# Kernel tuning notes

Hardware: AMD Instinct MI355X
Metric: run time of the kernel (lower is better)

Reference implementation:

```python
import jax, jax.numpy as jnp
import numpy as np
from jax import lax

MU = 255
H = 64            # block_hidden_size
SKIP = 256        # skip_size
NUM_LAYERS = 24
CYCLE = 6
UP_CONV = 4       # upsample_convs=[4]
UP_REPEAT = 75
LF = 80           # local_features_size
B = 2
L = 64            # local feature frames
T = L * UP_CONV * UP_REPEAT  # 19200 signal samples


def setup_inputs() -> dict:
    key = jax.random.key(0)
    ks = jax.random.split(key, 16)
    r = lambda k, shape, sc=0.05: jax.random.normal(k, shape, jnp.float32) * sc
    return {
        "local_features": jax.random.normal(ks[0], (B, L, LF), jnp.float32),
        "gold_signal": jax.random.uniform(ks[1], (B, T), jnp.float32, minval=-1.0, maxval=1.0),
        "embed_w": r(ks[2], (H, 1)),
        "embed_b": r(ks[3], (H,)),
        "up_w": r(ks[4], (LF, LF, UP_CONV)),
        "up_b": r(ks[5], (LF,)),
        "proj_w": r(ks[6], (NUM_LAYERS * 2 * H, LF)),
        "proj_b": r(ks[7], (NUM_LAYERS * 2 * H,)),
        "dil_w": r(ks[8], (NUM_LAYERS, 2 * H, H, 2)),
        "dil_b": r(ks[9], (NUM_LAYERS, 2 * H)),
        "skip_w": r(ks[10], (NUM_LAYERS, SKIP, H)),
        "skip_b": r(ks[11], (NUM_LAYERS, SKIP)),
        "res_w": r(ks[12], (NUM_LAYERS - 1, H, H)),
        "res_b": r(ks[13], (NUM_LAYERS - 1, H)),
        "out1_w": r(ks[14], (MU + 1, SKIP)),
        "out2_w": r(ks[15], (MU + 1, MU + 1)),
    }


def _causal_dilated_conv(x, w, b, dilation):
    # x: [B, C, T]; w: [O, C, 2]; left-pad so output[t] depends on inputs <= t
    xp = jnp.pad(x, ((0, 0), (0, 0), (dilation, 0)))
    y = lax.conv_general_dilated(xp, w, window_strides=(1,), padding="VALID",
                                 rhs_dilation=(dilation,),
                                 dimension_numbers=("NCH", "OIH", "NCH"))
    return y + b[None, :, None]


def _upsample(local_features, up_w, up_b, proj_w, proj_b):
    # local_features: [B, L, LF] -> cond [B, NUM_LAYERS, 2H, T]
    x = jnp.transpose(local_features, (0, 2, 1))  # [B, LF, L]
    # ConvTranspose1d with kernel_size == stride == UP_CONV (no overlap)
    y = jnp.einsum("bfl,fgk->bglk", x, up_w).reshape(x.shape[0], LF, -1)
    y = y + up_b[None, :, None]                                  # [B, LF, L*4]
    # 1x1 projection to per-layer gate conditioning (chunking in the original
    # is a memory trick, math-identical to a single conv)
    z = jnp.einsum("bft,of->bot", y, proj_w) + proj_b[None, :, None]
    z = jnp.repeat(z, UP_REPEAT, axis=-1)                        # [B, NL*2H, T]
    return z.reshape(z.shape[0], NUM_LAYERS, 2 * H, -1)


def reference(local_features, gold_signal, embed_w, embed_b, up_w, up_b,
              proj_w, proj_b, dil_w, dil_b, skip_w, skip_b, res_w, res_b,
              out1_w, out2_w):
    cond = _upsample(local_features, up_w, up_b, proj_w, proj_b)
    # embed: Conv1d(1 -> H, kernel 1)
    x = gold_signal[:, None, :] * embed_w[None, :, :] + embed_b[None, :, None]
    skip_sum = None
    for i in range(NUM_LAYERS):
        dilation = 2 ** (i % CYCLE)
        y = _causal_dilated_conv(x, dil_w[i], dil_b[i], dilation) + cond[:, i]
        gated = jnp.tanh(y[:, :H]) * jax.nn.sigmoid(y[:, H:])
        skip = jnp.einsum("bht,sh->bst", gated, skip_w[i]) + skip_b[i][None, :, None]
        skip_sum = skip if skip_sum is None else skip_sum + skip
        if i < NUM_LAYERS - 1:  # last layer has no residual out_conv
            x = x + jnp.einsum("bht,oh->bot", gated, res_w[i]) + res_b[i][None, :, None]
    h = jnp.einsum("bst,os->bot", jax.nn.relu(skip_sum), out1_w)
    h = jnp.einsum("bst,os->bot", jax.nn.relu(h), out2_w)
    return jax.nn.log_softmax(h, axis=1)  # [B, MU+1, T]
```

## Files before the change

kernel.cpp:

```cpp
#include <hip/hip_runtime.h>
#include <math.h>

#define T_TOT 19200
#define HD    64
#define SKIPN 256
#define NLAYER 24
#define LFN   80
#define NB    2
#define NTL   128
#define HALO  64
#define XR    (NTL + HALO)
#define NGT   (T_TOT / NTL)
#define NOH   32
#define NTH   (T_TOT / NOH)
#define NCH   (T_TOT / 32)

typedef float  f32x4  __attribute__((ext_vector_type(4)));
typedef __bf16 bf16x8 __attribute__((ext_vector_type(8)));
typedef __bf16 bf16x4 __attribute__((ext_vector_type(4)));

__device__ __forceinline__ f32x4 mfma16(bf16x8 a, bf16x8 b, f32x4 c) {
    return __builtin_amdgcn_mfma_f32_16x16x32_bf16(a, b, c, 0, 0, 0);
}

__global__ __launch_bounds__(256) void prep_kernel(
    const float* __restrict__ dil_w, const float* __restrict__ skip_w,
    const float* __restrict__ skip_b, const float* __restrict__ res_w,
    const float* __restrict__ out1_w, const float* __restrict__ out2_w,
    __bf16* __restrict__ A1f, __bf16* __restrict__ Asf, __bf16* __restrict__ A3f,
    __bf16* __restrict__ Ao1f, __bf16* __restrict__ Ao2f, float* __restrict__ sbsum)
{
    int idx = blockIdx.x * 256 + threadIdx.x;
    if (idx < 24 * 128 * 128) {
        {
            int j = idx & 7, lane = (idx >> 3) & 63, ks = (idx >> 9) & 3;
            int mt = (idx >> 11) & 7, l = idx >> 14;
            int row = mt * 16 + (lane & 15);
            int k   = ks * 32 + (lane >> 4) * 8 + j;
            A1f[idx] = (__bf16)dil_w[((l * 128 + row) * 64 + (k & 63)) * 2 + (k >> 6)];
        }
        {
            int j = idx & 7, lane = (idx >> 3) & 63, ks = (idx >> 9) & 1;
            int mt = (idx >> 10) & 15, l = idx >> 14;
            int row = mt * 16 + (lane & 15);
            int k   = ks * 32 + (lane >> 4) * 8 + j;
            Asf[idx] = (__bf16)skip_w[(l * 256 + row) * 64 + k];
        }
    }
    if (idx < 23 * 64 * 64) {
        int j = idx & 7, lane = (idx >> 3) & 63, ks = (idx >> 9) & 1;
        int mt = (idx >> 10) & 3, l = idx >> 12;
        int row = mt * 16 + (lane & 15);
        int k   = ks * 32 + (lane >> 4) * 8 + j;
        A3f[idx] = (__bf16)res_w[(l * 64 + row) * 64 + k];
    }
    if (idx < 256 * 256) {
        int j = idx & 7, lane = (idx >> 3) & 63, ks = (idx >> 9) & 7;
        int mt = idx >> 12;
        int row = mt * 16 + (lane & 15);
        int k   = ks * 32 + (lane >> 4) * 8 + j;
        Ao1f[idx] = (__bf16)out1_w[row * 256 + k];
        Ao2f[idx] = (__bf16)out2_w[row * 256 + k];
    }
    if (idx < 256) {
        float s = 0.0f;
        #pragma unroll
        for (int l = 0; l < NLAYER; ++l) s += skip_b[l * 256 + idx];
        sbsum[idx] = s;
    }
}

__global__ __launch_bounds__(256) void up_kernel(
    const float* __restrict__ lf, const float* __restrict__ up_w,
    const float* __restrict__ up_b, float* __restrict__ y_up)
{
    int idx = blockIdx.x * 256 + threadIdx.x;
    if (idx >= NB * LFN * 256) return;
    int t4 = idx & 255;
    int g  = (idx >> 8) % LFN;
    int b  = idx / (LFN * 256);
    int l = t4 >> 2, k = t4 & 3;
    float acc = up_b[g];
    const float* lfp = lf + (b * 64 + l) * LFN;
    #pragma unroll 8
    for (int f = 0; f < LFN; ++f)
        acc += lfp[f] * up_w[(f * LFN + g) * 4 + k];
    y_up[idx] = acc;
}

__global__ __launch_bounds__(256) void proj_kernel(
    const float* __restrict__ y_up, const float* __restrict__ proj_w,
    const float* __restrict__ proj_b, float* __restrict__ z)
{
    int idx = blockIdx.x * 256 + threadIdx.x;
    if (idx >= NB * 3072 * 256) return;
    int t4 = idx & 255;
    int o  = (idx >> 8) % 3072;
    int b  = idx / (3072 * 256);
    float acc = proj_b[o];
    const float* yp = y_up + b * LFN * 256 + t4;
    const float* wp = proj_w + o * LFN;
    #pragma unroll 8
    for (int g = 0; g < LFN; ++g)
        acc += wp[g] * yp[g * 256];
    z[idx] = acc;
}

__global__ __launch_bounds__(512, 4) void layer_group(
    const float* __restrict__ gold, const float* __restrict__ ew,
    const float* __restrict__ eb,
    const __bf16* __restrict__ xg_in, __bf16* __restrict__ xg_out,
    const float* __restrict__ zbuf, const float* __restrict__ dil_b,
    const float* __restrict__ res_b,
    const __bf16* __restrict__ A1f, const __bf16* __restrict__ A3f,
    __bf16* __restrict__ G, int L0, int first, int last)
{
    __shared__ __bf16 xh[XR][72];
    __shared__ __bf16 Gs[XR][72];
    __shared__ float  zs[4][128];

    const int b    = blockIdx.y;
    const int tb   = blockIdx.x;
    const int t0   = tb * NTL;
    const int tid  = threadIdx.x;
    const int lane = tid & 63;
    const int w    = tid >> 6;
    const int wm   = w & 3;
    const int wg   = w >> 2;
    const int n16  = lane & 15;
    const int quad = lane >> 4;
    const int q0   = ((t0 - HALO > 0) ? t0 - HALO : 0) / 75;

    bf16x8 z8;
    #pragma unroll
    for (int u = 0; u < 8; ++u) z8[u] = (__bf16)0.0f;

    if (first) {
        for (int idx = tid; idx < XR * 8; idx += 512) {
            int r = idx >> 3, hc = (idx & 7) * 8;
            int t = t0 - HALO + r;
            bf16x8 v = z8;
            if (t >= 0) {
                float gv = gold[b * T_TOT + t];
                #pragma unroll
                for (int u = 0; u < 8; ++u)
                    v[u] = (__bf16)(gv * ew[hc + u] + eb[hc + u]);
            }
            *(bf16x8*)&xh[r][hc] = v;
        }
    } else {
        for (int idx = tid; idx < XR * 8; idx += 512) {
            int r = idx >> 3, hc = (idx & 7) * 8;
            int t = t0 - HALO + r;
            bf16x8 v = (t >= 0)
                ? *(const bf16x8*)&xg_in[((size_t)b * T_TOT + t) * 64 + hc] : z8;
            *(bf16x8*)&xh[r][hc] = v;
        }
    }

    const bf16x8* A1v = (const bf16x8*)A1f;
    const bf16x8* A3v = (const bf16x8*)A3f;
    f32x4 zero4 = {0.0f, 0.0f, 0.0f, 0.0f};

    for (int j = 0; j < 6; ++j) {
        const int l = L0 + j;
        const int d = 1 << j;

        if (tid < 512) {
            int qq = tid >> 7, o = tid & 127;
            int q = q0 + qq; if (q > 255) q = 255;
            zs[qq][o] = dil_b[l * 128 + o] +
                        zbuf[((size_t)(b * 3072 + l * 128 + o)) * 256 + q];
        }
        bf16x8 a1a[4], a1b[4];
        #pragma unroll
        for (int ks = 0; ks < 4; ++ks) {
            a1a[ks] = A1v[((l * 8 + wm) * 4 + ks) * 64 + lane];
            a1b[ks] = A1v[((l * 8 + 4 + wm) * 4 + ks) * 64 + lane];
        }
        __syncthreads();

        #pragma unroll
        for (int nt0 = 0; nt0 < 6; ++nt0) {
            int nt = wg * 6 + nt0;
            int nn = nt * 16 + n16;
            int rm = (nn >= d) ? nn - d : 0;
            bf16x8 b0 = *(const bf16x8*)&xh[rm][quad * 8];
            bf16x8 b1 = *(const bf16x8*)&xh[rm][32 + quad * 8];
            bf16x8 b2 = *(const bf16x8*)&xh[nn][quad * 8];
            bf16x8 b3 = *(const bf16x8*)&xh[nn][32 + quad * 8];
            f32x4 aa = zero4, ab = zero4;
            aa = mfma16(a1a[0], b0, aa); ab = mfma16(a1b[0], b0, ab);
            aa = mfma16(a1a[1], b1, aa); ab = mfma16(a1b[1], b1, ab);
            aa = mfma16(a1a[2], b2, aa); ab = mfma16(a1b[2], b2, ab);
            aa = mfma16(a1a[3], b3, aa); ab = mfma16(a1b[3], b3, ab);

            int tt = t0 - HALO + nn;
            int qq = ((tt > 0) ? tt : 0) / 75 - q0;
            bf16x4 g4;
            #pragma unroll
            for (int r = 0; r < 4; ++r) {
                int o = wm * 16 + quad * 4 + r;
                float ya = aa[r] + zs[qq][o];
                float yb = ab[r] + zs[qq][o + 64];
                float th = 1.0f - 2.0f * __builtin_amdgcn_rcpf(__expf(2.0f * ya) + 1.0f);
                float sg = __builtin_amdgcn_rcpf(1.0f + __expf(-yb));
                g4[r] = (__bf16)(th * sg);
            }
            *(bf16x4*)&Gs[nn][wm * 16 + quad * 4] = g4;
        }
        __syncthreads();

        {
            __bf16* Gl = G + (((size_t)(b * NCH + tb * 4)) * NLAYER + l) * 2048;
            for (int idx = tid; idx < 128 * 8; idx += 512) {
                int rr = idx >> 3, hc = (idx & 7) * 8;
                size_t off = (size_t)(rr >> 5) * (NLAYER * 2048) + (rr & 31) * 64 + hc;
                *(bf16x8*)&Gl[off] = *(const bf16x8*)&Gs[HALO + rr][hc];
            }
        }

        if (l < NLAYER - 1) {
            bf16x8 a3[2];
            #pragma unroll
            for (int ks = 0; ks < 2; ++ks)
                a3[ks] = A3v[((l * 4 + wm) * 2 + ks) * 64 + lane];
            int o0 = wm * 16 + quad * 4;
            f32x4 rb = *(const f32x4*)&res_b[l * 64 + o0];
            #pragma unroll
            for (int nt0 = 0; nt0 < 6; ++nt0) {
                int nn = (wg * 6 + nt0) * 16 + n16;
                bf16x8 g0 = *(const bf16x8*)&Gs[nn][quad * 8];
                bf16x8 g1 = *(const bf16x8*)&Gs[nn][32 + quad * 8];
                f32x4 ar = zero4;
                ar = mfma16(a3[0], g0, ar);
                ar = mfma16(a3[1], g1, ar);
                bf16x4 xo = *(const bf16x4*)&xh[nn][o0];
                bf16x4 xn;
                #pragma unroll
                for (int r = 0; r < 4; ++r)
                    xn[r] = (__bf16)((float)xo[r] + ar[r] + rb[r]);
                *(bf16x4*)&xh[nn][o0] = xn;
            }
        }
    }

    if (!last) {
        __syncthreads();
        for (int idx = tid; idx < 128 * 8; idx += 512) {
            int rr = idx >> 3, hc = (idx & 7) * 8;
            *(bf16x8*)&xg_out[((size_t)b * T_TOT + t0 + rr) * 64 + hc] =
                *(const bf16x8*)&xh[HALO + rr][hc];
        }
    }
}

__global__ __launch_bounds__(256, 4) void head_mfma(
    const __bf16* __restrict__ G, const __bf16* __restrict__ Asf,
    const float* __restrict__ sbsum, const __bf16* __restrict__ Ao1f,
    const __bf16* __restrict__ Ao2f, float* __restrict__ out)
{
    __shared__ __bf16 Vs[NOH][264];
    __shared__ float redm[4][2][16];
    __shared__ float reds[4][2][16];

    const int b    = blockIdx.y;
    const int tcb  = blockIdx.x;
    const int t0   = tcb * NOH;
    const int tid  = threadIdx.x;
    const int lane = tid & 63;
    const int w    = tid >> 6;
    const int n16  = lane & 15;
    const int quad = lane >> 4;

    f32x4 zero4 = {0.0f, 0.0f, 0.0f, 0.0f};
    f32x4 acc[4][2];
    #pragma unroll
    for (int mt = 0; mt < 4; ++mt)
        #pragma unroll
        for (int nt = 0; nt < 2; ++nt) acc[mt][nt] = zero4;

    const bf16x8* Asv = (const bf16x8*)Asf;
    const __bf16* Gc  = G + ((size_t)(b * NCH + tcb)) * (NLAYER * 2048);

    for (int l = 0; l < NLAYER; ++l) {
        const __bf16* Gl = Gc + l * 2048;
        #pragma unroll
        for (int ks = 0; ks < 2; ++ks) {
            bf16x8 bfr[2];
            #pragma unroll
            for (int nt = 0; nt < 2; ++nt)
                bfr[nt] = *(const bf16x8*)&Gl[(nt * 16 + n16) * 64 + ks * 32 + quad * 8];
            #pragma unroll
            for (int mt = 0; mt < 4; ++mt) {
                bf16x8 af = Asv[((l * 16 + w * 4 + mt) * 2 + ks) * 64 + lane];
                #pragma unroll
                for (int nt = 0; nt < 2; ++nt)
                    acc[mt][nt] = mfma16(af, bfr[nt], acc[mt][nt]);
            }
        }
    }
    {
        int s0 = w * 64 + quad * 4;
        #pragma unroll
        for (int mt = 0; mt < 4; ++mt)
            #pragma unroll
            for (int nt = 0; nt < 2; ++nt) {
                bf16x4 v4;
                #pragma unroll
                for (int r = 0; r < 4; ++r)
                    v4[r] = (__bf16)fmaxf(acc[mt][nt][r] + sbsum[s0 + mt * 16 + r], 0.0f);
                *(bf16x4*)&Vs[nt * 16 + n16][s0 + mt * 16] = v4;
            }
    }
    __syncthreads();

    const bf16x8* W1v = (const bf16x8*)Ao1f;
    const bf16x8* W2v = (const bf16x8*)Ao2f;

    #pragma unroll
    for (int mt = 0; mt < 4; ++mt)
        #pragma unroll
        for (int nt = 0; nt < 2; ++nt) acc[mt][nt] = zero4;
    #pragma unroll
    for (int ks = 0; ks < 8; ++ks) {
        bf16x8 bfr[2];
        #pragma unroll
        for (int nt = 0; nt < 2; ++nt)
            bfr[nt] = *(const bf16x8*)&Vs[nt * 16 + n16][ks * 32 + quad * 8];
        #pragma unroll
        for (int mt = 0; mt < 4; ++mt) {
            bf16x8 af = W1v[((w * 4 + mt) * 8 + ks) * 64 + lane];
            #pragma unroll
            for (int nt = 0; nt < 2; ++nt)
                acc[mt][nt] = mfma16(af, bfr[nt], acc[mt][nt]);
        }
    }
    __syncthreads();
    #pragma unroll
    for (int mt = 0; mt < 4; ++mt)
        #pragma unroll
        for (int nt = 0; nt < 2; ++nt) {
            int o0 = w * 64 + mt * 16 + quad * 4;
            bf16x4 v4;
            #pragma unroll
            for (int r = 0; r < 4; ++r)
                v4[r] = (__bf16)fmaxf(acc[mt][nt][r], 0.0f);
            *(bf16x4*)&Vs[nt * 16 + n16][o0] = v4;
        }
    __syncthreads();

    #pragma unroll
    for (int mt = 0; mt < 4; ++mt)
        #pragma unroll
        for (int nt = 0; nt < 2; ++nt) acc[mt][nt] = zero4;
    #pragma unroll
    for (int ks = 0; ks < 8; ++ks) {
        bf16x8 bfr[2];
        #pragma unroll
        for (int nt = 0; nt < 2; ++nt)
            bfr[nt] = *(const bf16x8*)&Vs[nt * 16 + n16][ks * 32 + quad * 8];
        #pragma unroll
        for (int mt = 0; mt < 4; ++mt) {
            bf16x8 af = W2v[((w * 4 + mt) * 8 + ks) * 64 + lane];
            #pragma unroll
            for (int nt = 0; nt < 2; ++nt)
                acc[mt][nt] = mfma16(af, bfr[nt], acc[mt][nt]);
        }
    }

    float lmax[2], lsum[2];
    #pragma unroll
    for (int nt = 0; nt < 2; ++nt) {
        float m = -1e30f;
        #pragma unroll
        for (int mt = 0; mt < 4; ++mt)
            #pragma unroll
            for (int r = 0; r < 4; ++r) m = fmaxf(m, acc[mt][nt][r]);
        m = fmaxf(m, __shfl_xor(m, 16, 64));
        m = fmaxf(m, __shfl_xor(m, 32, 64));
        lmax[nt] = m;
    }
    if (quad == 0) {
        #pragma unroll
        for (int nt = 0; nt < 2; ++nt) redm[w][nt][n16] = lmax[nt];
    }
    __syncthreads();
    #pragma unroll
    for (int nt = 0; nt < 2; ++nt) {
        float m = redm[0][nt][n16];
        m = fmaxf(m, redm[1][nt][n16]);
        m = fmaxf(m, redm[2][nt][n16]);
        m = fmaxf(m, redm[3][nt][n16]);
        lmax[nt] = m;
        float s = 0.0f;
        #pragma unroll
        for (int mt = 0; mt < 4; ++mt)
            #pragma unroll
            for (int r = 0; r < 4; ++r) s += __expf(acc[mt][nt][r] - m);
        s += __shfl_xor(s, 16, 64);
        s += __shfl_xor(s, 32, 64);
        lsum[nt] = s;
    }
    if (quad == 0) {
        #pragma unroll
        for (int nt = 0; nt < 2; ++nt) reds[w][nt][n16] = lsum[nt];
    }
    __syncthreads();
    #pragma unroll
    for (int nt = 0; nt < 2; ++nt) {
        float s = reds[0][nt][n16] + reds[1][nt][n16] +
                  reds[2][nt][n16] + reds[3][nt][n16];
        float lse = lmax[nt] + logf(s);
        int t = t0 + nt * 16 + n16;
        #pragma unroll
        for (int mt = 0; mt < 4; ++mt)
            #pragma unroll
            for (int r = 0; r < 4; ++r) {
                int o = w * 64 + mt * 16 + quad * 4 + r;
                out[((size_t)(b * SKIPN + o)) * T_TOT + t] = acc[mt][nt][r] - lse;
            }
    }
}

extern "C" void kernel_launch(void* const* d_in, const int* in_sizes, int n_in,
                              void* d_out, int out_size, void* d_ws, size_t ws_size,
                              hipStream_t stream) {
    const float* lf       = (const float*)d_in[0];
    const float* gold     = (const float*)d_in[1];
    const float* embed_w  = (const float*)d_in[2];
    const float* embed_b  = (const float*)d_in[3];
    const float* up_w     = (const float*)d_in[4];
    const float* up_b     = (const float*)d_in[5];
    const float* proj_w   = (const float*)d_in[6];
    const float* proj_b   = (const float*)d_in[7];
    const float* dil_w    = (const float*)d_in[8];
    const float* dil_b    = (const float*)d_in[9];
    const float* skip_w   = (const float*)d_in[10];
    const float* skip_b   = (const float*)d_in[11];
    const float* res_w    = (const float*)d_in[12];
    const float* res_b    = (const float*)d_in[13];
    const float* out1_w   = (const float*)d_in[14];
    const float* out2_w   = (const float*)d_in[15];

    __bf16* A1f  = (__bf16*)d_ws;
    __bf16* Asf  = A1f + 393216;
    __bf16* A3f  = Asf + 393216;
    __bf16* Ao1f = A3f + 94208;
    __bf16* Ao2f = Ao1f + 65536;
    __bf16* G    = Ao2f + 65536;
    __bf16* xga  = G + (size_t)NB * NCH * NLAYER * 2048;
    __bf16* xgb  = xga + (size_t)NB * T_TOT * HD;
    float*  sbsum = (float*)(xgb + (size_t)NB * T_TOT * HD);
    float*  y_up  = sbsum + 256;
    float*  zbuf  = y_up + NB * LFN * 256;

    prep_kernel<<<(24 * 128 * 128 + 255) / 256, 256, 0, stream>>>(
        dil_w, skip_w, skip_b, res_w, out1_w, out2_w,
        A1f, Asf, A3f, Ao1f, Ao2f, sbsum);
    up_kernel  <<<(NB * LFN * 256 + 255) / 256, 256, 0, stream>>>(lf, up_w, up_b, y_up);
    proj_kernel<<<(NB * 3072 * 256) / 256,      256, 0, stream>>>(y_up, proj_w, proj_b, zbuf);

    const __bf16* xin[4] = { xga, xga, xgb, xga };
    __bf16*       xout[4] = { xga, xgb, xga, xgb };
    for (int g = 0; g < 4; ++g) {
        layer_group<<<dim3(NGT, NB), 512, 0, stream>>>(
            gold, embed_w, embed_b, xin[g], xout[g],
            zbuf, dil_b, res_b, A1f, A3f, G,
            6 * g, (g == 0) ? 1 : 0, (g == 3) ? 1 : 0);
    }

    head_mfma<<<dim3(NTH, NB), 256, 0, stream>>>(G, Asf, sbsum, Ao1f, Ao2f, (float*)d_out);
}
```

Baseline: 382.5 us.

## Shrink layer tiles, skip unneeded halo rows, transpose conditioning, prefetch head G

Halves the time tile per layer block to 64 outputs with 256 threads, so there are more blocks. Each layer skips the halo row tiles that can no longer influence valid outputs, based on the cumulative dilation. A new transpose kernel pre-adds the dilation bias and stores conditioning as time-major, so the per-layer z loads are contiguous. The head kernel double-buffers G fragments across layers. The cost is a larger halo-to-output ratio, meaning more redundant halo compute per output row, plus one extra launch and buffer.

New measurement: 391.2 us. 2.3% more time.

```diff
diff --git a/kernel.cpp b/kernel.cpp
--- a/kernel.cpp
+++ b/kernel.cpp
@@ -7,7 +7,7 @@
 #define NLAYER 24
 #define LFN   80
 #define NB    2
-#define NTL   128
+#define NTL   64
 #define HALO  64
 #define XR    (NTL + HALO)
 #define NGT   (T_TOT / NTL)
@@ -106,18 +106,41 @@
     z[idx] = acc;
 }
 
-__global__ __launch_bounds__(512, 4) void layer_group(
+__global__ __launch_bounds__(256) void ztrans_kernel(
+    const float* __restrict__ z, const float* __restrict__ dil_b,
+    float* __restrict__ zt)
+{
+    __shared__ float tile[32][33];
+    const int b  = blockIdx.z;
+    const int o0 = blockIdx.x * 32;
+    const int q0 = blockIdx.y * 32;
+    const int tx = threadIdx.x & 31;
+    const int ty = threadIdx.x >> 5;
+    #pragma unroll
+    for (int k = 0; k < 4; ++k) {
+        int o = o0 + ty + k * 8;
+        tile[ty + k * 8][tx] = z[((size_t)(b * 3072 + o)) * 256 + q0 + tx];
+    }
+    __syncthreads();
+    #pragma unroll
+    for (int k = 0; k < 4; ++k) {
+        int q = q0 + ty + k * 8;
+        int o = o0 + tx;
+        zt[((size_t)(b * 256 + q)) * 3072 + o] = tile[tx][ty + k * 8] + dil_b[o];
+    }
+}
+
+__global__ __launch_bounds__(256, 3) void layer_group(
     const float* __restrict__ gold, const float* __restrict__ ew,
     const float* __restrict__ eb,
     const __bf16* __restrict__ xg_in, __bf16* __restrict__ xg_out,
-    const float* __restrict__ zbuf, const float* __restrict__ dil_b,
-    const float* __restrict__ res_b,
+    const float* __restrict__ zt, const float* __restrict__ res_b,
     const __bf16* __restrict__ A1f, const __bf16* __restrict__ A3f,
     __bf16* __restrict__ G, int L0, int first, int last)
 {
     __shared__ __bf16 xh[XR][72];
     __shared__ __bf16 Gs[XR][72];
-    __shared__ float  zs[4][128];
+    __shared__ float  zs[3][128];
 
     const int b    = blockIdx.y;
     const int tb   = blockIdx.x;
@@ -125,8 +148,6 @@
     const int tid  = threadIdx.x;
     const int lane = tid & 63;
     const int w    = tid >> 6;
-    const int wm   = w & 3;
-    const int wg   = w >> 2;
     const int n16  = lane & 15;
     const int quad = lane >> 4;
     const int q0   = ((t0 - HALO > 0) ? t0 - HALO : 0) / 75;
@@ -136,7 +157,7 @@
     for (int u = 0; u < 8; ++u) z8[u] = (__bf16)0.0f;
 
     if (first) {
-        for (int idx = tid; idx < XR * 8; idx += 512) {
+        for (int idx = tid; idx < XR * 8; idx += 256) {
             int r = idx >> 3, hc = (idx & 7) * 8;
             int t = t0 - HALO + r;
             bf16x8 v = z8;
@@ -149,7 +170,7 @@
             *(bf16x8*)&xh[r][hc] = v;
         }
     } else {
-        for (int idx = tid; idx < XR * 8; idx += 512) {
+        for (int idx = tid; idx < XR * 8; idx += 256) {
             int r = idx >> 3, hc = (idx & 7) * 8;
             int t = t0 - HALO + r;
             bf16x8 v = (t >= 0)
@@ -161,28 +182,26 @@
     const bf16x8* A1v = (const bf16x8*)A1f;
     const bf16x8* A3v = (const bf16x8*)A3f;
     f32x4 zero4 = {0.0f, 0.0f, 0.0f, 0.0f};
+    const int stj[6] = {0, 0, 0, 1, 2, 4};
 
     for (int j = 0; j < 6; ++j) {
         const int l = L0 + j;
         const int d = 1 << j;
 
-        if (tid < 512) {
-            int qq = tid >> 7, o = tid & 127;
+        for (int idx = tid; idx < 384; idx += 256) {
+            int qq = idx >> 7, oo = idx & 127;
             int q = q0 + qq; if (q > 255) q = 255;
-            zs[qq][o] = dil_b[l * 128 + o] +
-                        zbuf[((size_t)(b * 3072 + l * 128 + o)) * 256 + q];
+            zs[qq][oo] = zt[((size_t)(b * 256 + q)) * 3072 + l * 128 + oo];
         }
         bf16x8 a1a[4], a1b[4];
         #pragma unroll
         for (int ks = 0; ks < 4; ++ks) {
-            a1a[ks] = A1v[((l * 8 + wm) * 4 + ks) * 64 + lane];
-            a1b[ks] = A1v[((l * 8 + 4 + wm) * 4 + ks) * 64 + lane];
+            a1a[ks] = A1v[((l * 8 + w) * 4 + ks) * 64 + lane];
+            a1b[ks] = A1v[((l * 8 + 4 + w) * 4 + ks) * 64 + lane];
         }
         __syncthreads();
 
-        #pragma unroll
-        for (int nt0 = 0; nt0 < 6; ++nt0) {
-            int nt = wg * 6 + nt0;
+        for (int nt = stj[j]; nt < 8; ++nt) {
             int nn = nt * 16 + n16;
             int rm = (nn >= d) ? nn - d : 0;
             bf16x8 b0 = *(const bf16x8*)&xh[rm][quad * 8];
@@ -197,39 +216,38 @@
 
             int tt = t0 - HALO + nn;
             int qq = ((tt > 0) ? tt : 0) / 75 - q0;
+            int o0 = w * 16 + quad * 4;
+            f32x4 za = *(const f32x4*)&zs[qq][o0];
+            f32x4 zb = *(const f32x4*)&zs[qq][o0 + 64];
             bf16x4 g4;
             #pragma unroll
             for (int r = 0; r < 4; ++r) {
-                int o = wm * 16 + quad * 4 + r;
-                float ya = aa[r] + zs[qq][o];
-                float yb = ab[r] + zs[qq][o + 64];
+                float ya = aa[r] + za[r];
+                float yb = ab[r] + zb[r];
                 float th = 1.0f - 2.0f * __builtin_amdgcn_rcpf(__expf(2.0f * ya) + 1.0f);
                 float sg = __builtin_amdgcn_rcpf(1.0f + __expf(-yb));
                 g4[r] = (__bf16)(th * sg);
             }
-            *(bf16x4*)&Gs[nn][wm * 16 + quad * 4] = g4;
+            *(bf16x4*)&Gs[nn][o0] = g4;
         }
         __syncthreads();
 
-        {
-            __bf16* Gl = G + (((size_t)(b * NCH + tb * 4)) * NLAYER + l) * 2048;
-            for (int idx = tid; idx < 128 * 8; idx += 512) {
-                int rr = idx >> 3, hc = (idx & 7) * 8;
-                size_t off = (size_t)(rr >> 5) * (NLAYER * 2048) + (rr & 31) * 64 + hc;
-                *(bf16x8*)&Gl[off] = *(const bf16x8*)&Gs[HALO + rr][hc];
-            }
+        for (int idx = tid; idx < 512; idx += 256) {
+            int rr = idx >> 3, hc = (idx & 7) * 8;
+            int cb = tb * 2 + (rr >> 5);
+            size_t off = ((size_t)(b * NCH + cb) * NLAYER + l) * 2048 + (rr & 31) * 64 + hc;
+            *(bf16x8*)&G[off] = *(const bf16x8*)&Gs[HALO + rr][hc];
         }
 
         if (l < NLAYER - 1) {
             bf16x8 a3[2];
             #pragma unroll
             for (int ks = 0; ks < 2; ++ks)
-                a3[ks] = A3v[((l * 4 + wm) * 2 + ks) * 64 + lane];
-            int o0 = wm * 16 + quad * 4;
+                a3[ks] = A3v[((l * 4 + w) * 2 + ks) * 64 + lane];
+            int o0 = w * 16 + quad * 4;
             f32x4 rb = *(const f32x4*)&res_b[l * 64 + o0];
-            #pragma unroll
-            for (int nt0 = 0; nt0 < 6; ++nt0) {
-                int nn = (wg * 6 + nt0) * 16 + n16;
+            for (int nt = stj[j]; nt < 8; ++nt) {
+                int nn = nt * 16 + n16;
                 bf16x8 g0 = *(const bf16x8*)&Gs[nn][quad * 8];
                 bf16x8 g1 = *(const bf16x8*)&Gs[nn][32 + quad * 8];
                 f32x4 ar = zero4;
@@ -247,7 +265,7 @@
 
     if (!last) {
         __syncthreads();
-        for (int idx = tid; idx < 128 * 8; idx += 512) {
+        for (int idx = tid; idx < 512; idx += 256) {
             int rr = idx >> 3, hc = (idx & 7) * 8;
             *(bf16x8*)&xg_out[((size_t)b * T_TOT + t0 + rr) * 64 + hc] =
                 *(const bf16x8*)&xh[HALO + rr][hc];
@@ -281,24 +299,34 @@
         for (int nt = 0; nt < 2; ++nt) acc[mt][nt] = zero4;
 
     const bf16x8* Asv = (const bf16x8*)Asf;
-    const __bf16* Gc  = G + ((size_t)(b * NCH + tcb)) * (NLAYER * 2048);
-
+    const __bf16* Gl  = G + ((size_t)(b * NCH + tcb)) * (NLAYER * 2048);
+
+    bf16x8 gb[4], gn[4];
+    #pragma unroll
+    for (int p = 0; p < 4; ++p) {
+        int ks = p >> 1, nt = p & 1;
+        gb[p] = *(const bf16x8*)&Gl[(nt * 16 + n16) * 64 + ks * 32 + quad * 8];
+    }
     for (int l = 0; l < NLAYER; ++l) {
-        const __bf16* Gl = Gc + l * 2048;
-        #pragma unroll
-        for (int ks = 0; ks < 2; ++ks) {
-            bf16x8 bfr[2];
-            #pragma unroll
-            for (int nt = 0; nt < 2; ++nt)
-                bfr[nt] = *(const bf16x8*)&Gl[(nt * 16 + n16) * 64 + ks * 32 + quad * 8];
+        if (l < NLAYER - 1) {
+            const __bf16* Gn = Gl + 2048;
+            #pragma unroll
+            for (int p = 0; p < 4; ++p) {
+                int ks = p >> 1, nt = p & 1;
+                gn[p] = *(const bf16x8*)&Gn[(nt * 16 + n16) * 64 + ks * 32 + quad * 8];
+            }
+        }
+        #pragma unroll
+        for (int ks = 0; ks < 2; ++ks)
             #pragma unroll
             for (int mt = 0; mt < 4; ++mt) {
                 bf16x8 af = Asv[((l * 16 + w * 4 + mt) * 2 + ks) * 64 + lane];
-                #pragma unroll
-                for (int nt = 0; nt < 2; ++nt)
-                    acc[mt][nt] = mfma16(af, bfr[nt], acc[mt][nt]);
-            }
-        }
+                acc[mt][0] = mfma16(af, gb[ks * 2 + 0], acc[mt][0]);
+                acc[mt][1] = mfma16(af, gb[ks * 2 + 1], acc[mt][1]);
+            }
+        #pragma unroll
+        for (int p = 0; p < 4; ++p) gb[p] = gn[p];
+        Gl += 2048;
     }
     {
         int s0 = w * 64 + quad * 4;
@@ -453,20 +481,22 @@
     __bf16* xgb  = xga + (size_t)NB * T_TOT * HD;
     float*  sbsum = (float*)(xgb + (size_t)NB * T_TOT * HD);
     float*  y_up  = sbsum + 256;
-    float*  zbuf  = y_up + NB * LFN * 256;
+    float*  z     = y_up + NB * LFN * 256;
+    float*  zt    = z + NB * 3072 * 256;
 
     prep_kernel<<<(24 * 128 * 128 + 255) / 256, 256, 0, stream>>>(
         dil_w, skip_w, skip_b, res_w, out1_w, out2_w,
         A1f, Asf, A3f, Ao1f, Ao2f, sbsum);
     up_kernel  <<<(NB * LFN * 256 + 255) / 256, 256, 0, stream>>>(lf, up_w, up_b, y_up);
-    proj_kernel<<<(NB * 3072 * 256) / 256,      256, 0, stream>>>(y_up, proj_w, proj_b, zbuf);
+    proj_kernel<<<(NB * 3072 * 256) / 256,      256, 0, stream>>>(y_up, proj_w, proj_b, z);
+    ztrans_kernel<<<dim3(96, 8, NB), 256, 0, stream>>>(z, dil_b, zt);
 
     const __bf16* xin[4] = { xga, xga, xgb, xga };
     __bf16*       xout[4] = { xga, xgb, xga, xgb };
     for (int g = 0; g < 4; ++g) {
-        layer_group<<<dim3(NGT, NB), 512, 0, stream>>>(
+        layer_group<<<dim3(NGT, NB), 256, 0, stream>>>(
             gold, embed_w, embed_b, xin[g], xout[g],
-            zbuf, dil_b, res_b, A1f, A3f, G,
+            zt, res_b, A1f, A3f, G,
             6 * g, (g == 0) ? 1 : 0, (g == 3) ? 1 : 0);
     }
 
```

## Transpose conditioning buffer and widen head tile to 64 timesteps with 8 waves

Applied to the files above, without the earlier changes.

Adds a transpose kernel that folds dil_b into the projected conditioning and stores it time-major, so layer_group's per-layer zs load becomes coalesced and the gate step reads it as vector loads. The head kernel now processes 64 timesteps per block with 512 threads, with each wave covering 2 M-tiles by 4 N-tiles. This halves the number of head blocks and reuses each weight fragment across more columns. The cost is an extra kernel launch, an extra transposed buffer, and fewer, larger head blocks with an 8-way reduction.

Result: slower. 443.2 us (+15.9%).

```diff
diff --git a/kernel.cpp b/kernel.cpp
--- a/kernel.cpp
+++ b/kernel.cpp
@@ -11,7 +11,7 @@
 #define HALO  64
 #define XR    (NTL + HALO)
 #define NGT   (T_TOT / NTL)
-#define NOH   32
+#define NOH   64
 #define NTH   (T_TOT / NOH)
 #define NCH   (T_TOT / 32)
 
@@ -106,12 +106,35 @@
     z[idx] = acc;
 }
 
+__global__ __launch_bounds__(256) void ztrans_kernel(
+    const float* __restrict__ z, const float* __restrict__ dil_b,
+    float* __restrict__ zt)
+{
+    __shared__ float tile[32][33];
+    const int b  = blockIdx.z;
+    const int o0 = blockIdx.x * 32;
+    const int q0 = blockIdx.y * 32;
+    const int tx = threadIdx.x & 31;
+    const int ty = threadIdx.x >> 5;
+    #pragma unroll
+    for (int k = 0; k < 4; ++k) {
+        int o = o0 + ty + k * 8;
+        tile[ty + k * 8][tx] = z[((size_t)(b * 3072 + o)) * 256 + q0 + tx];
+    }
+    __syncthreads();
+    #pragma unroll
+    for (int k = 0; k < 4; ++k) {
+        int q = q0 + ty + k * 8;
+        int o = o0 + tx;
+        zt[((size_t)(b * 256 + q)) * 3072 + o] = tile[tx][ty + k * 8] + dil_b[o];
+    }
+}
+
 __global__ __launch_bounds__(512, 4) void layer_group(
     const float* __restrict__ gold, const float* __restrict__ ew,
     const float* __restrict__ eb,
     const __bf16* __restrict__ xg_in, __bf16* __restrict__ xg_out,
-    const float* __restrict__ zbuf, const float* __restrict__ dil_b,
-    const float* __restrict__ res_b,
+    const float* __restrict__ zt, const float* __restrict__ res_b,
     const __bf16* __restrict__ A1f, const __bf16* __restrict__ A3f,
     __bf16* __restrict__ G, int L0, int first, int last)
 {
@@ -166,11 +189,10 @@
         const int l = L0 + j;
         const int d = 1 << j;
 
-        if (tid < 512) {
-            int qq = tid >> 7, o = tid & 127;
+        {
+            int qq = tid >> 7, oo = tid & 127;
             int q = q0 + qq; if (q > 255) q = 255;
-            zs[qq][o] = dil_b[l * 128 + o] +
-                        zbuf[((size_t)(b * 3072 + l * 128 + o)) * 256 + q];
+            zs[qq][oo] = zt[((size_t)(b * 256 + q)) * 3072 + l * 128 + oo];
         }
         bf16x8 a1a[4], a1b[4];
         #pragma unroll
@@ -197,17 +219,19 @@
 
             int tt = t0 - HALO + nn;
             int qq = ((tt > 0) ? tt : 0) / 75 - q0;
+            int o0 = wm * 16 + quad * 4;
+            f32x4 za = *(const f32x4*)&zs[qq][o0];
+            f32x4 zb = *(const f32x4*)&zs[qq][o0 + 64];
             bf16x4 g4;
             #pragma unroll
             for (int r = 0; r < 4; ++r) {
-                int o = wm * 16 + quad * 4 + r;
-                float ya = aa[r] + zs[qq][o];
-                float yb = ab[r] + zs[qq][o + 64];
+                float ya = aa[r] + za[r];
+                float yb = ab[r] + zb[r];
                 float th = 1.0f - 2.0f * __builtin_amdgcn_rcpf(__expf(2.0f * ya) + 1.0f);
                 float sg = __builtin_amdgcn_rcpf(1.0f + __expf(-yb));
                 g4[r] = (__bf16)(th * sg);
             }
-            *(bf16x4*)&Gs[nn][wm * 16 + quad * 4] = g4;
+            *(bf16x4*)&Gs[nn][o0] = g4;
         }
         __syncthreads();
 
@@ -255,18 +279,18 @@
     }
 }
 
-__global__ __launch_bounds__(256, 4) void head_mfma(
+__global__ __launch_bounds__(512, 2) void head_mfma(
     const __bf16* __restrict__ G, const __bf16* __restrict__ Asf,
     const float* __restrict__ sbsum, const __bf16* __restrict__ Ao1f,
     const __bf16* __restrict__ Ao2f, float* __restrict__ out)
 {
     __shared__ __bf16 Vs[NOH][264];
-    __shared__ float redm[4][2][16];
-    __shared__ float reds[4][2][16];
+    __shared__ float redm[8][4][16];
+    __shared__ float reds[8][4][16];
 
     const int b    = blockIdx.y;
-    const int tcb  = blockIdx.x;
-    const int t0   = tcb * NOH;
+    const int xb   = blockIdx.x;
+    const int t0   = xb * NOH;
     const int tid  = threadIdx.x;
     const int lane = tid & 63;
     const int w    = tid >> 6;
@@ -274,44 +298,49 @@
     const int quad = lane >> 4;
 
     f32x4 zero4 = {0.0f, 0.0f, 0.0f, 0.0f};
-    f32x4 acc[4][2];
-    #pragma unroll
-    for (int mt = 0; mt < 4; ++mt)
-        #pragma unroll
-        for (int nt = 0; nt < 2; ++nt) acc[mt][nt] = zero4;
+    f32x4 acc[2][4];
+    #pragma unroll
+    for (int mt = 0; mt < 2; ++mt)
+        #pragma unroll
+        for (int nt = 0; nt < 4; ++nt) acc[mt][nt] = zero4;
 
     const bf16x8* Asv = (const bf16x8*)Asf;
-    const __bf16* Gc  = G + ((size_t)(b * NCH + tcb)) * (NLAYER * 2048);
+    const __bf16* Gc0 = G + ((size_t)(b * NCH + xb * 2) * NLAYER) * 2048;
+    const __bf16* Gc1 = Gc0 + (size_t)NLAYER * 2048;
 
     for (int l = 0; l < NLAYER; ++l) {
-        const __bf16* Gl = Gc + l * 2048;
+        bf16x8 bfr[2][4];
         #pragma unroll
         for (int ks = 0; ks < 2; ++ks) {
-            bf16x8 bfr[2];
-            #pragma unroll
-            for (int nt = 0; nt < 2; ++nt)
-                bfr[nt] = *(const bf16x8*)&Gl[(nt * 16 + n16) * 64 + ks * 32 + quad * 8];
-            #pragma unroll
-            for (int mt = 0; mt < 4; ++mt) {
-                bf16x8 af = Asv[((l * 16 + w * 4 + mt) * 2 + ks) * 64 + lane];
+            #pragma unroll
+            for (int nt = 0; nt < 4; ++nt) {
+                const __bf16* base = ((nt < 2) ? Gc0 : Gc1) + l * 2048;
+                bfr[ks][nt] = *(const bf16x8*)
+                    &base[((nt & 1) * 16 + n16) * 64 + ks * 32 + quad * 8];
+            }
+        }
+        #pragma unroll
+        for (int ks = 0; ks < 2; ++ks)
+            #pragma unroll
+            for (int mt = 0; mt < 2; ++mt) {
+                bf16x8 af = Asv[((l * 16 + w * 2 + mt) * 2 + ks) * 64 + lane];
                 #pragma unroll
-                for (int nt = 0; nt < 2; ++nt)
-                    acc[mt][nt] = mfma16(af, bfr[nt], acc[mt][nt]);
-            }
-        }
-    }
-    {
-        int s0 = w * 64 + quad * 4;
-        #pragma unroll
-        for (int mt = 0; mt < 4; ++mt)
-            #pragma unroll
-            for (int nt = 0; nt < 2; ++nt) {
-                bf16x4 v4;
-                #pragma unroll
-                for (int r = 0; r < 4; ++r)
-                    v4[r] = (__bf16)fmaxf(acc[mt][nt][r] + sbsum[s0 + mt * 16 + r], 0.0f);
-                *(bf16x4*)&Vs[nt * 16 + n16][s0 + mt * 16] = v4;
-            }
+                for (int nt = 0; nt < 4; ++nt)
+                    acc[mt][nt] = mfma16(af, bfr[ks][nt], acc[mt][nt]);
+            }
+    }
+    #pragma unroll
+    for (int mt = 0; mt < 2; ++mt) {
+        int s0 = (w * 2 + mt) * 16 + quad * 4;
+        f32x4 sb = *(const f32x4*)&sbsum[s0];
+        #pragma unroll
+        for (int nt = 0; nt < 4; ++nt) {
+            bf16x4 v4;
+            #pragma unroll
+            for (int r = 0; r < 4; ++r)
+                v4[r] = (__bf16)fmaxf(acc[mt][nt][r] + sb[r], 0.0f);
+            *(bf16x4*)&Vs[nt * 16 + n16][s0] = v4;
+        }
     }
     __syncthreads();
 
@@ -319,62 +348,63 @@
     const bf16x8* W2v = (const bf16x8*)Ao2f;
 
     #pragma unroll
-    for (int mt = 0; mt < 4; ++mt)
-        #pragma unroll
-        for (int nt = 0; nt < 2; ++nt) acc[mt][nt] = zero4;
+    for (int mt = 0; mt < 2; ++mt)
+        #pragma unroll
+        for (int nt = 0; nt < 4; ++nt) acc[mt][nt] = zero4;
     #pragma unroll
     for (int ks = 0; ks < 8; ++ks) {
-        bf16x8 bfr[2];
-        #pragma unroll
-        for (int nt = 0; nt < 2; ++nt)
+        bf16x8 bfr[4];
+        #pragma unroll
+        for (int nt = 0; nt < 4; ++nt)
             bfr[nt] = *(const bf16x8*)&Vs[nt * 16 + n16][ks * 32 + quad * 8];
         #pragma unroll
-        for (int mt = 0; mt < 4; ++mt) {
-            bf16x8 af = W1v[((w * 4 + mt) * 8 + ks) * 64 + lane];
-            #pragma unroll
-            for (int nt = 0; nt < 2; ++nt)
+        for (int mt = 0; mt < 2; ++mt) {
+            bf16x8 af = W1v[((w * 2 + mt) * 8 + ks) * 64 + lane];
+            #pragma unroll
+            for (int nt = 0; nt < 4; ++nt)
                 acc[mt][nt] = mfma16(af, bfr[nt], acc[mt][nt]);
         }
     }
     __syncthreads();
     #pragma unroll
-    for (int mt = 0; mt < 4; ++mt)
-        #pragma unroll
-        for (int nt = 0; nt < 2; ++nt) {
-            int o0 = w * 64 + mt * 16 + quad * 4;
+    for (int mt = 0; mt < 2; ++mt) {
+        int o0 = (w * 2 + mt) * 16 + quad * 4;
+        #pragma unroll
+        for (int nt = 0; nt < 4; ++nt) {
             bf16x4 v4;
             #pragma unroll
             for (int r = 0; r < 4; ++r)
                 v4[r] = (__bf16)fmaxf(acc[mt][nt][r], 0.0f);
             *(bf16x4*)&Vs[nt * 16 + n16][o0] = v4;
         }
+    }
     __syncthreads();
 
     #pragma unroll
-    for (int mt = 0; mt < 4; ++mt)
-        #pragma unroll
-        for (int nt = 0; nt < 2; ++nt) acc[mt][nt] = zero4;
+    for (int mt = 0; mt < 2; ++mt)
+        #pragma unroll
+        for (int nt = 0; nt < 4; ++nt) acc[mt][nt] = zero4;
     #pragma unroll
     for (int ks = 0; ks < 8; ++ks) {
-        bf16x8 bfr[2];
-        #pragma unroll
-        for (int nt = 0; nt < 2; ++nt)
+        bf16x8 bfr[4];
+        #pragma unroll
+        for (int nt = 0; nt < 4; ++nt)
             bfr[nt] = *(const bf16x8*)&Vs[nt * 16 + n16][ks * 32 + quad * 8];
         #pragma unroll
-        for (int mt = 0; mt < 4; ++mt) {
-            bf16x8 af = W2v[((w * 4 + mt) * 8 + ks) * 64 + lane];
-            #pragma unroll
-            for (int nt = 0; nt < 2; ++nt)
+        for (int mt = 0; mt < 2; ++mt) {
+            bf16x8 af = W2v[((w * 2 + mt) * 8 + ks) * 64 + lane];
+            #pragma unroll
+            for (int nt = 0; nt < 4; ++nt)
                 acc[mt][nt] = mfma16(af, bfr[nt], acc[mt][nt]);
         }
     }
 
-    float lmax[2], lsum[2];
-    #pragma unroll
-    for (int nt = 0; nt < 2; ++nt) {
+    float lmax[4], lsum[4];
+    #pragma unroll
+    for (int nt = 0; nt < 4; ++nt) {
         float m = -1e30f;
         #pragma unroll
-        for (int mt = 0; mt < 4; ++mt)
+        for (int mt = 0; mt < 2; ++mt)
             #pragma unroll
             for (int r = 0; r < 4; ++r) m = fmaxf(m, acc[mt][nt][r]);
         m = fmaxf(m, __shfl_xor(m, 16, 64));
@@ -383,19 +413,18 @@
     }
     if (quad == 0) {
         #pragma unroll
-        for (int nt = 0; nt < 2; ++nt) redm[w][nt][n16] = lmax[nt];
+        for (int nt = 0; nt < 4; ++nt) redm[w][nt][n16] = lmax[nt];
     }
     __syncthreads();
     #pragma unroll
-    for (int nt = 0; nt < 2; ++nt) {
+    for (int nt = 0; nt < 4; ++nt) {
         float m = redm[0][nt][n16];
-        m = fmaxf(m, redm[1][nt][n16]);
-        m = fmaxf(m, redm[2][nt][n16]);
-        m = fmaxf(m, redm[3][nt][n16]);
+        #pragma unroll
+        for (int ww = 1; ww < 8; ++ww) m = fmaxf(m, redm[ww][nt][n16]);
         lmax[nt] = m;
         float s = 0.0f;
         #pragma unroll
-        for (int mt = 0; mt < 4; ++mt)
+        for (int mt = 0; mt < 2; ++mt)
             #pragma unroll
             for (int r = 0; r < 4; ++r) s += __expf(acc[mt][nt][r] - m);
         s += __shfl_xor(s, 16, 64);
@@ -404,20 +433,21 @@
     }
     if (quad == 0) {
         #pragma unroll
-        for (int nt = 0; nt < 2; ++nt) reds[w][nt][n16] = lsum[nt];
+        for (int nt = 0; nt < 4; ++nt) reds[w][nt][n16] = lsum[nt];
     }
     __syncthreads();
     #pragma unroll
-    for (int nt = 0; nt < 2; ++nt) {
-        float s = reds[0][nt][n16] + reds[1][nt][n16] +
-                  reds[2][nt][n16] + reds[3][nt][n16];
+    for (int nt = 0; nt < 4; ++nt) {
+        float s = reds[0][nt][n16];
+        #pragma unroll
+        for (int ww = 1; ww < 8; ++ww) s += reds[ww][nt][n16];
         float lse = lmax[nt] + logf(s);
         int t = t0 + nt * 16 + n16;
         #pragma unroll
-        for (int mt = 0; mt < 4; ++mt)
+        for (int mt = 0; mt < 2; ++mt)
             #pragma unroll
             for (int r = 0; r < 4; ++r) {
-                int o = w * 64 + mt * 16 + quad * 4 + r;
+                int o = (w * 2 + mt) * 16 + quad * 4 + r;
                 out[((size_t)(b * SKIPN + o)) * T_TOT + t] = acc[mt][nt][r] - lse;
             }
     }
@@ -453,22 +483,24 @@
     __bf16* xgb  = xga + (size_t)NB * T_TOT * HD;
     float*  sbsum = (float*)(xgb + (size_t)NB * T_TOT * HD);
     float*  y_up  = sbsum + 256;
-    float*  zbuf  = y_up + NB * LFN * 256;
+    float*  z     = y_up + NB * LFN * 256;
+    float*  zt    = z + NB * 3072 * 256;
 
     prep_kernel<<<(24 * 128 * 128 + 255) / 256, 256, 0, stream>>>(
         dil_w, skip_w, skip_b, res_w, out1_w, out2_w,
         A1f, Asf, A3f, Ao1f, Ao2f, sbsum);
     up_kernel  <<<(NB * LFN * 256 + 255) / 256, 256, 0, stream>>>(lf, up_w, up_b, y_up);
-    proj_kernel<<<(NB * 3072 * 256) / 256,      256, 0, stream>>>(y_up, proj_w, proj_b, zbuf);
+    proj_kernel<<<(NB * 3072 * 256) / 256,      256, 0, stream>>>(y_up, proj_w, proj_b, z);
+    ztrans_kernel<<<dim3(96, 8, NB), 256, 0, stream>>>(z, dil_b, zt);
 
     const __bf16* xin[4] = { xga, xga, xgb, xga };
     __bf16*       xout[4] = { xga, xgb, xga, xgb };
     for (int g = 0; g < 4; ++g) {
         layer_group<<<dim3(NGT, NB), 512, 0, stream>>>(
             gold, embed_w, embed_b, xin[g], xout[g],
-            zbuf, dil_b, res_b, A1f, A3f, G,
+            zt, res_b, A1f, A3f, G,
             6 * g, (g == 0) ? 1 : 0, (g == 3) ? 1 : 0);
     }
 
-    head_mfma<<<dim3(NTH, NB), 256, 0, stream>>>(G, Asf, sbsum, Ao1f, Ao2f, (float*)d_out);
-}
+    head_mfma<<<dim3(NTH, NB), 512, 0, stream>>>(G, Asf, sbsum, Ao1f, Ao2f, (float*)d_out);
+}
```
